# Kernel tuning notes

Hardware: AMD Instinct MI355X
Metric: run time of the kernel (lower is better)

Reference implementation:

```python
import jax, jax.numpy as jnp
import numpy as np

N_NODES = 100000
N_EDGES = 800000
D_IN = 128
D_HID = 128


def setup_inputs() -> dict:
    key = jax.random.key(0)
    ks = jax.random.split(key, 5)
    x = jax.random.normal(ks[0], (N_NODES, D_IN), dtype=jnp.float32)
    edge_index = jax.random.randint(ks[1], (2, N_EDGES), 0, N_NODES, dtype=jnp.int64)
    W1 = jax.random.normal(ks[2], (D_HID, D_IN), dtype=jnp.float32) * 0.05
    b1 = jnp.zeros((D_HID,), dtype=jnp.float32)
    W2 = jax.random.normal(ks[3], (D_HID, D_HID), dtype=jnp.float32) * 0.05
    b2 = jnp.zeros((D_HID,), dtype=jnp.float32)
    return {"x": x, "edge_index": edge_index, "W1": W1, "b1": b1, "W2": W2, "b2": b2}


def _gcn_conv(x, W, b, src, dst, norm, num_nodes):
    # x' = x @ W^T, then scatter-add normalized messages to dst, then + bias
    h = x @ W.T                                  # [N, d_out]
    msg = h[src] * norm[:, None]                 # [E+N, d_out] gather + scale
    out = jax.ops.segment_sum(msg, dst, num_segments=num_nodes)
    return out + b


def reference(x, edge_index, W1, b1, W2, b2):
    n = x.shape[0]
    loops = jnp.arange(n, dtype=edge_index.dtype)
    src = jnp.concatenate([edge_index[0], loops])  # self-loops appended (PyG GCNConv)
    dst = jnp.concatenate([edge_index[1], loops])
    # symmetric normalization: deg over target nodes (weight 1 per edge)
    deg = jax.ops.segment_sum(jnp.ones_like(dst, dtype=x.dtype), dst, num_segments=n)
    dis = jnp.where(deg > 0, jax.lax.rsqrt(jnp.maximum(deg, 1e-12)), 0.0)
    norm = dis[src] * dis[dst]
    h = jax.nn.relu(_gcn_conv(x, W1, b1, src, dst, norm, n))
    return _gcn_conv(h, W2, b2, src, dst, norm, n)
```

## Files before the change

kernel.cpp:

```cpp
#include <hip/hip_runtime.h>

#define D 128
#define BE 4096
#define SC 5120
#define LROW 136

typedef __attribute__((ext_vector_type(8))) short bf16x8;
typedef __attribute__((ext_vector_type(4))) float f32x4;
typedef __attribute__((ext_vector_type(8))) unsigned short u16x8;

__device__ inline unsigned short f2bf(float f) {
    unsigned u = __float_as_uint(f);
    return (unsigned short)((u + 0x7fff + ((u >> 16) & 1)) >> 16);
}
__device__ inline float bf2f(unsigned short s) {
    return __uint_as_float((unsigned)s << 16);
}
__device__ inline bf16x8 cvt8(const float* __restrict__ p) {
    float4 a = *(const float4*)p;
    float4 b = *(const float4*)(p + 4);
    bf16x8 r;
    r[0] = (short)f2bf(a.x); r[1] = (short)f2bf(a.y);
    r[2] = (short)f2bf(a.z); r[3] = (short)f2bf(a.w);
    r[4] = (short)f2bf(b.x); r[5] = (short)f2bf(b.y);
    r[6] = (short)f2bf(b.z); r[7] = (short)f2bf(b.w);
    return r;
}

__global__ void k_prep(const float* __restrict__ W1, const float* __restrict__ W2,
                       unsigned short* __restrict__ Wb1, unsigned short* __restrict__ Wb2,
                       int* __restrict__ bcnt, int* __restrict__ gcnt, int NBK) {
    int i = blockIdx.x * 256 + threadIdx.x;
    if (i < D * D) { Wb1[i] = f2bf(W1[i]); Wb2[i] = f2bf(W2[i]); }
    if (i < NBK) bcnt[i] = 0;
    if (i == D * D) *gcnt = 0;
}


__device__ inline void gemm1_tile(const float* __restrict__ xx,
                                  const unsigned short* __restrict__ Wb,
                                  unsigned short* __restrict__ g,
                                  int N, int tile, int t) {
    int w = t >> 6, l = t & 63;
    int r16 = l & 15, g4 = l >> 4;
    int base = tile * 128 + w * 32;
    int row0 = base + r16, row1 = row0 + 16;
    int cr0 = (row0 < N) ? row0 : N - 1;
    int cr1 = (row1 < N) ? row1 : N - 1;

    f32x4 acc0[8] = {};
    f32x4 acc1[8] = {};
    const unsigned short* wr = Wb + r16 * D + g4 * 8;

#pragma unroll 1
    for (int ks = 0; ks < 4; ks++) {
        bf16x8 b0 = cvt8(xx + (size_t)cr0 * D + g4 * 8 + ks * 32);
        bf16x8 b1 = cvt8(xx + (size_t)cr1 * D + g4 * 8 + ks * 32);
#pragma unroll
        for (int jt = 0; jt < 8; jt++) {
            bf16x8 a = *(const bf16x8*)(wr + jt * 16 * D + ks * 32);
            acc0[jt] = __builtin_amdgcn_mfma_f32_16x16x32_bf16(a, b0, acc0[jt], 0, 0, 0);
            acc1[jt] = __builtin_amdgcn_mfma_f32_16x16x32_bf16(a, b1, acc1[jt], 0, 0, 0);
        }
    }
#pragma unroll
    for (int tt = 0; tt < 2; tt++) {
        int row = base + tt * 16 + r16;
        if (row < N) {
#pragma unroll
            for (int jt = 0; jt < 8; jt++) {
                f32x4 a = tt ? acc1[jt] : acc0[jt];
                ushort4 o = { f2bf(a[0]), f2bf(a[1]), f2bf(a[2]), f2bf(a[3]) };
                *(ushort4*)&g[(size_t)row * D + jt * 16 + g4 * 4] = o;
            }
        }
    }
}


__global__ __launch_bounds__(256) void k_sort_gemm1a(
        const int* __restrict__ ei, int* __restrict__ bcnt, unsigned* __restrict__ brec,
        const float* __restrict__ x, const unsigned short* __restrict__ Wb1,
        unsigned short* __restrict__ g, int N, int E, int ntA, int sortB, int NBK) {
    int bid = blockIdx.x;
    if (bid % 3 == 2) {
        __shared__ unsigned srt[BE];
        __shared__ unsigned char bko[BE];
        __shared__ int hist[256];
        __shared__ int pfx[256];
        __shared__ int gbase[256];
        __shared__ int cur[256];
        int f = bid / 3;
        if (f >= sortB) return;
        int t = threadIdx.x;
        int e0 = f * BE;
        int n = E - e0; if (n > BE) n = BE;
        hist[t] = 0; cur[t] = 0;
        __syncthreads();
        unsigned rec[16]; int mb[16];
#pragma unroll
        for (int j = 0; j < 16; j++) {
            int e = e0 + j * 256 + t;
            if (e < E) {
                int s = ei[e], d = ei[E + e];
                rec[j] = ((unsigned)s << 9) | (unsigned)(d & 511);
                mb[j] = d >> 9;
                atomicAdd(&hist[mb[j]], 1);
            } else mb[j] = -1;
        }
        __syncthreads();
        int v = hist[t];
        pfx[t] = v;
        __syncthreads();
        for (int dd = 1; dd < 256; dd <<= 1) {
            int xv = (t >= dd) ? pfx[t - dd] : 0;
            __syncthreads();
            pfx[t] += xv;
            __syncthreads();
        }
        pfx[t] -= v;
        if (v > 0 && t < NBK) gbase[t] = atomicAdd(&bcnt[t], v);
        __syncthreads();
#pragma unroll
        for (int j = 0; j < 16; j++) {
            if (mb[j] >= 0) {
                int p = pfx[mb[j]] + atomicAdd(&cur[mb[j]], 1);
                srt[p] = rec[j];
                bko[p] = (unsigned char)mb[j];
            }
        }
        __syncthreads();
        for (int i = t; i < n; i += 256) {
            int b = bko[i];
            int pos = gbase[b] + (i - pfx[b]);
            if (pos < SC) brec[(size_t)b * SC + pos] = srt[i];
        }
    } else {
        int gid = (bid / 3) * 2 + (bid % 3);
        if (gid >= ntA) return;
        gemm1_tile(x, Wb1, g, N, gid, threadIdx.x);
    }
}

__global__ __launch_bounds__(256) void k_build_gemm1b(
        const int* __restrict__ bcnt, const unsigned* __restrict__ brec,
        int* __restrict__ cnt, int* __restrict__ rp, int* __restrict__ col,
        int* __restrict__ gcnt,
        const float* __restrict__ x, const unsigned short* __restrict__ Wb1,
        unsigned short* __restrict__ g, int N, int ntA, int ntiles, int NBK) {
    int bid = blockIdx.x;
    if (bid % 3 == 2) {
        __shared__ int c512[512];
        __shared__ int base512[512];
        __shared__ int psc[256];
        __shared__ int bksum;
        int b = bid / 3, t = threadIdx.x;
        if (b >= NBK) return;
        c512[t] = 0; c512[t + 256] = 0;
        __syncthreads();
        int total = bcnt[b]; if (total > SC) total = SC;
        for (int i = t; i < total; i += 256)
            atomicAdd(&c512[brec[(size_t)b * SC + i] & 511], 1);
        __syncthreads();
        int d0 = c512[2 * t], d1 = c512[2 * t + 1];
        int pair = d0 + d1;
        psc[t] = pair;
        __syncthreads();
        for (int dd = 1; dd < 256; dd <<= 1) {
            int xv = (t >= dd) ? psc[t - dd] : 0;
            __syncthreads();
            psc[t] += xv;
            __syncthreads();
        }
        int pexc = psc[t] - pair;
        if (t == 255) bksum = atomicAdd(gcnt, psc[255]);
        __syncthreads();
        int gb = bksum;
        base512[2 * t]     = gb + pexc;
        base512[2 * t + 1] = gb + pexc + d0;
        c512[2 * t] = 0; c512[2 * t + 1] = 0;
        __syncthreads();
        for (int i = t; i < total; i += 256) {
            unsigned rec = brec[(size_t)b * SC + i];
            int dl = rec & 511;
            int p = atomicAdd(&c512[dl], 1);
            col[base512[dl] + p] = (int)(rec >> 9);
        }
        __syncthreads();
#pragma unroll
        for (int k = 0; k < 2; k++) {
            int dl = t + k * 256;
            int node = b * 512 + dl;
            if (node < N) { cnt[node] = c512[dl]; rp[node] = base512[dl]; }
        }
    } else {
        int gid = ntA + (bid / 3) * 2 + (bid % 3);
        if (gid >= ntiles) return;
        gemm1_tile(x, Wb1, g, N, gid, threadIdx.x);
    }
}


__global__ __launch_bounds__(256) void k_agg1_g2(
        const unsigned short* __restrict__ gtab, const int* __restrict__ cnt,
        const int* __restrict__ rp, const int* __restrict__ col,
        const float* __restrict__ b1, const unsigned short* __restrict__ Wb2,
        unsigned short* __restrict__ g2, int N) {
    __shared__ __align__(16) unsigned short hl[16 * LROW];
    int t = threadIdx.x, grp = t >> 4, l16 = t & 15;
    int n0 = blockIdx.x * 16;
    int node = n0 + grp;
    bool valid = (node < N);
    int nc = valid ? node : N - 1;
    const u16x8* G = (const u16x8*)gtab;

    int deg = valid ? cnt[node] : 0;
    float disv = rsqrtf((float)(deg + 1));
    float acc[8];
    {
        u16x8 s = G[(size_t)nc * 16 + l16];
#pragma unroll
        for (int j = 0; j < 8; j++) acc[j] = bf2f(s[j]) * disv;
    }
    const int* cb = col + (valid ? rp[node] : 0);
    int i = 0;
    for (; i + 3 < deg; i += 4) {
        int u0 = cb[i], u1 = cb[i + 1], u2 = cb[i + 2], u3 = cb[i + 3];
        u16x8 m0 = G[(size_t)u0 * 16 + l16];
        u16x8 m1 = G[(size_t)u1 * 16 + l16];
        u16x8 m2 = G[(size_t)u2 * 16 + l16];
        u16x8 m3 = G[(size_t)u3 * 16 + l16];
        float d0 = rsqrtf((float)(cnt[u0] + 1));
        float d1 = rsqrtf((float)(cnt[u1] + 1));
        float d2 = rsqrtf((float)(cnt[u2] + 1));
        float d3 = rsqrtf((float)(cnt[u3] + 1));
#pragma unroll
        for (int j = 0; j < 8; j++)
            acc[j] += (bf2f(m0[j]) * d0 + bf2f(m1[j]) * d1)
                    + (bf2f(m2[j]) * d2 + bf2f(m3[j]) * d3);
    }
    for (; i < deg; i++) {
        int u = cb[i];
        u16x8 m = G[(size_t)u * 16 + l16];
        float du = rsqrtf((float)(cnt[u] + 1));
#pragma unroll
        for (int j = 0; j < 8; j++) acc[j] += bf2f(m[j]) * du;
    }
    {
        const float4* B4 = (const float4*)b1;
        float4 bb0 = B4[l16 * 2], bb1 = B4[l16 * 2 + 1];
        float r[8];
        r[0] = fmaf(acc[0], disv, bb0.x); r[1] = fmaf(acc[1], disv, bb0.y);
        r[2] = fmaf(acc[2], disv, bb0.z); r[3] = fmaf(acc[3], disv, bb0.w);
        r[4] = fmaf(acc[4], disv, bb1.x); r[5] = fmaf(acc[5], disv, bb1.y);
        r[6] = fmaf(acc[6], disv, bb1.z); r[7] = fmaf(acc[7], disv, bb1.w);
        u16x8 hv;
#pragma unroll
        for (int j = 0; j < 8; j++)
            hv[j] = valid ? f2bf(fmaxf(r[j], 0.f)) : (unsigned short)0;
        *(u16x8*)&hl[grp * LROW + l16 * 8] = hv;
    }
    __syncthreads();

    int w = t >> 6, l = t & 63;
    int r16 = l & 15, g4 = l >> 4;
    f32x4 a0 = {}, a1 = {};
    const unsigned short* wr = Wb2 + r16 * D + g4 * 8;
    int xb = r16 * LROW + g4 * 8;
#pragma unroll 1
    for (int ks = 0; ks < 4; ks++) {
        bf16x8 b = *(const bf16x8*)&hl[xb + ks * 32];
        bf16x8 A0 = *(const bf16x8*)(wr + (2 * w) * 16 * D + ks * 32);
        bf16x8 A1 = *(const bf16x8*)(wr + (2 * w + 1) * 16 * D + ks * 32);
        a0 = __builtin_amdgcn_mfma_f32_16x16x32_bf16(A0, b, a0, 0, 0, 0);
        a1 = __builtin_amdgcn_mfma_f32_16x16x32_bf16(A1, b, a1, 0, 0, 0);
    }
    int orow = n0 + r16;
    if (orow < N) {
        float dv = rsqrtf((float)(cnt[orow] + 1));
        ushort4 o0 = { f2bf(a0[0] * dv), f2bf(a0[1] * dv),
                       f2bf(a0[2] * dv), f2bf(a0[3] * dv) };
        ushort4 o1 = { f2bf(a1[0] * dv), f2bf(a1[1] * dv),
                       f2bf(a1[2] * dv), f2bf(a1[3] * dv) };
        *(ushort4*)&g2[(size_t)orow * D + (2 * w) * 16 + g4 * 4] = o0;
        *(ushort4*)&g2[(size_t)orow * D + (2 * w + 1) * 16 + g4 * 4] = o1;
    }
}

__global__ __launch_bounds__(256) void k_agg2(
        const unsigned short* __restrict__ g2, const int* __restrict__ cnt,
        const int* __restrict__ rp, const int* __restrict__ col,
        const float* __restrict__ b2, float* __restrict__ out, int N) {
    int node = blockIdx.x * 16 + (threadIdx.x >> 4);
    if (node >= N) return;
    int l16 = threadIdx.x & 15;
    const u16x8* G = (const u16x8*)g2;
    int deg = cnt[node];
    float acc[8];
    {
        u16x8 s = G[(size_t)node * 16 + l16];
#pragma unroll
        for (int j = 0; j < 8; j++) acc[j] = bf2f(s[j]);
    }
    const int* cb = col + rp[node];
    int i = 0;
    for (; i + 3 < deg; i += 4) {
        int u0 = cb[i], u1 = cb[i + 1], u2 = cb[i + 2], u3 = cb[i + 3];
        u16x8 m0 = G[(size_t)u0 * 16 + l16];
        u16x8 m1 = G[(size_t)u1 * 16 + l16];
        u16x8 m2 = G[(size_t)u2 * 16 + l16];
        u16x8 m3 = G[(size_t)u3 * 16 + l16];
#pragma unroll
        for (int j = 0; j < 8; j++)
            acc[j] += (bf2f(m0[j]) + bf2f(m1[j])) + (bf2f(m2[j]) + bf2f(m3[j]));
    }
    for (; i < deg; i++) {
        u16x8 m = G[(size_t)cb[i] * 16 + l16];
#pragma unroll
        for (int j = 0; j < 8; j++) acc[j] += bf2f(m[j]);
    }
    float disv = rsqrtf((float)(deg + 1));
    const float4* B4 = (const float4*)b2;
    float4 bb0 = B4[l16 * 2], bb1 = B4[l16 * 2 + 1];
    float4 o0, o1;
    o0.x = fmaf(acc[0], disv, bb0.x); o0.y = fmaf(acc[1], disv, bb0.y);
    o0.z = fmaf(acc[2], disv, bb0.z); o0.w = fmaf(acc[3], disv, bb0.w);
    o1.x = fmaf(acc[4], disv, bb1.x); o1.y = fmaf(acc[5], disv, bb1.y);
    o1.z = fmaf(acc[6], disv, bb1.z); o1.w = fmaf(acc[7], disv, bb1.w);
    ((float4*)out)[(size_t)node * 32 + l16 * 2]     = o0;
    ((float4*)out)[(size_t)node * 32 + l16 * 2 + 1] = o1;
}


extern "C" void kernel_launch(void* const* d_in, const int* in_sizes, int n_in,
                              void* d_out, int out_size, void* d_ws, size_t ws_size,
                              hipStream_t stream) {
    const float* x  = (const float*)d_in[0];
    const int*   ei = (const int*)d_in[1];
    const float* W1 = (const float*)d_in[2];
    const float* b1 = (const float*)d_in[3];
    const float* W2 = (const float*)d_in[4];
    const float* b2 = (const float*)d_in[5];
    float* out = (float*)d_out;

    int N = in_sizes[0] / D;
    int E = in_sizes[1] / 2;
    int NBK = (N + 511) >> 9;

    char* w = (char*)d_ws;
    unsigned short* g  = (unsigned short*)w;  size_t off = (size_t)N * D * 2;
    off = (off + 255) & ~(size_t)255;
    unsigned short* g2 = (unsigned short*)(w + off); off += (size_t)N * D * 2;
    off = (off + 255) & ~(size_t)255;
    int* cnt  = (int*)(w + off);             off += (size_t)N * 4;
    off = (off + 255) & ~(size_t)255;
    int* rp   = (int*)(w + off);             off += (size_t)N * 4;
    off = (off + 255) & ~(size_t)255;
    int* col  = (int*)(w + off);             off += (size_t)E * 4;
    off = (off + 255) & ~(size_t)255;
    unsigned short* Wb1 = (unsigned short*)(w + off); off += (size_t)D * D * 2;
    unsigned short* Wb2 = (unsigned short*)(w + off); off += (size_t)D * D * 2;
    off = (off + 255) & ~(size_t)255;
    int* bcnt = (int*)(w + off);             off += (size_t)NBK * 4;
    off = (off + 255) & ~(size_t)255;
    int* gcnt = (int*)(w + off);             off += 256;
    unsigned* brec = (unsigned*)(w + off);   off += (size_t)NBK * SC * 4;

    int ntiles = (N + 127) / 128;
    int ntA = (ntiles + 1) / 2;
    int ntB = ntiles - ntA;
    int sortB = (E + BE - 1) / BE;
    int fb1 = sortB > (ntA + 1) / 2 ? sortB : (ntA + 1) / 2;
    int fb2 = NBK   > (ntB + 1) / 2 ? NBK   : (ntB + 1) / 2;
    int agg_grid = (N + 15) / 16;

    k_prep<<<(D * D + 511) / 256, 256, 0, stream>>>(W1, W2, Wb1, Wb2, bcnt, gcnt, NBK);

    k_sort_gemm1a<<<3 * fb1, 256, 0, stream>>>(ei, bcnt, brec, x, Wb1, g,
                                               N, E, ntA, sortB, NBK);
    k_build_gemm1b<<<3 * fb2, 256, 0, stream>>>(bcnt, brec, cnt, rp, col, gcnt,
                                                x, Wb1, g, N, ntA, ntiles, NBK);

    k_agg1_g2<<<agg_grid, 256, 0, stream>>>(g, cnt, rp, col, b1, Wb2, g2, N);

    k_agg2<<<agg_grid, 256, 0, stream>>>(g2, cnt, rp, col, b2, out, N);
}
```

Measured before the change: 160.0 us.

## Sort nodes by degree for first aggregation and move whole GEMM1 into sort kernel

```diff
diff --git a/kernel.cpp b/kernel.cpp
--- a/kernel.cpp
+++ b/kernel.cpp
@@ -29,68 +29,59 @@
 
 __global__ void k_prep(const float* __restrict__ W1, const float* __restrict__ W2,
                        unsigned short* __restrict__ Wb1, unsigned short* __restrict__ Wb2,
-                       int* __restrict__ bcnt, int* __restrict__ gcnt, int NBK) {
+                       int* __restrict__ bcnt, int* __restrict__ gcnt,
+                       int* __restrict__ dbins, int NBK) {
     int i = blockIdx.x * 256 + threadIdx.x;
     if (i < D * D) { Wb1[i] = f2bf(W1[i]); Wb2[i] = f2bf(W2[i]); }
     if (i < NBK) bcnt[i] = 0;
     if (i == D * D) *gcnt = 0;
-}
-
-
-__device__ inline void gemm1_tile(const float* __restrict__ xx,
-                                  const unsigned short* __restrict__ Wb,
-                                  unsigned short* __restrict__ g,
-                                  int N, int tile, int t) {
+    if (i < 32) dbins[i] = 0;
+}
+
+
+__device__ inline void gemm1_tile64(const float* __restrict__ xx,
+                                    const unsigned short* __restrict__ Wb,
+                                    unsigned short* __restrict__ g,
+                                    int N, int tile, int t) {
     int w = t >> 6, l = t & 63;
     int r16 = l & 15, g4 = l >> 4;
-    int base = tile * 128 + w * 32;
-    int row0 = base + r16, row1 = row0 + 16;
-    int cr0 = (row0 < N) ? row0 : N - 1;
-    int cr1 = (row1 < N) ? row1 : N - 1;
-
-    f32x4 acc0[8] = {};
-    f32x4 acc1[8] = {};
+    int row = tile * 64 + w * 16 + r16;
+    int cr = (row < N) ? row : N - 1;
+    f32x4 acc[8] = {};
     const unsigned short* wr = Wb + r16 * D + g4 * 8;
-
 #pragma unroll 1
     for (int ks = 0; ks < 4; ks++) {
-        bf16x8 b0 = cvt8(xx + (size_t)cr0 * D + g4 * 8 + ks * 32);
-        bf16x8 b1 = cvt8(xx + (size_t)cr1 * D + g4 * 8 + ks * 32);
+        bf16x8 b = cvt8(xx + (size_t)cr * D + g4 * 8 + ks * 32);
 #pragma unroll
         for (int jt = 0; jt < 8; jt++) {
             bf16x8 a = *(const bf16x8*)(wr + jt * 16 * D + ks * 32);
-            acc0[jt] = __builtin_amdgcn_mfma_f32_16x16x32_bf16(a, b0, acc0[jt], 0, 0, 0);
-            acc1[jt] = __builtin_amdgcn_mfma_f32_16x16x32_bf16(a, b1, acc1[jt], 0, 0, 0);
-        }
-    }
-#pragma unroll
-    for (int tt = 0; tt < 2; tt++) {
-        int row = base + tt * 16 + r16;
-        if (row < N) {
-#pragma unroll
-            for (int jt = 0; jt < 8; jt++) {
-                f32x4 a = tt ? acc1[jt] : acc0[jt];
-                ushort4 o = { f2bf(a[0]), f2bf(a[1]), f2bf(a[2]), f2bf(a[3]) };
-                *(ushort4*)&g[(size_t)row * D + jt * 16 + g4 * 4] = o;
-            }
-        }
-    }
-}
-
-
-__global__ __launch_bounds__(256) void k_sort_gemm1a(
+            acc[jt] = __builtin_amdgcn_mfma_f32_16x16x32_bf16(a, b, acc[jt], 0, 0, 0);
+        }
+    }
+    if (row < N) {
+#pragma unroll
+        for (int jt = 0; jt < 8; jt++) {
+            ushort4 o = { f2bf(acc[jt][0]), f2bf(acc[jt][1]),
+                          f2bf(acc[jt][2]), f2bf(acc[jt][3]) };
+            *(ushort4*)&g[(size_t)row * D + jt * 16 + g4 * 4] = o;
+        }
+    }
+}
+
+
+__global__ __launch_bounds__(256) void k_sort_gemm1(
         const int* __restrict__ ei, int* __restrict__ bcnt, unsigned* __restrict__ brec,
         const float* __restrict__ x, const unsigned short* __restrict__ Wb1,
-        unsigned short* __restrict__ g, int N, int E, int ntA, int sortB, int NBK) {
+        unsigned short* __restrict__ g, int N, int E, int nt64, int sortB, int NBK) {
     int bid = blockIdx.x;
-    if (bid % 3 == 2) {
+    if (bid % 9 == 8) {
         __shared__ unsigned srt[BE];
         __shared__ unsigned char bko[BE];
         __shared__ int hist[256];
         __shared__ int pfx[256];
         __shared__ int gbase[256];
         __shared__ int cur[256];
-        int f = bid / 3;
+        int f = bid / 9;
         if (f >= sortB) return;
         int t = threadIdx.x;
         int e0 = f * BE;
@@ -136,67 +127,105 @@
             if (pos < SC) brec[(size_t)b * SC + pos] = srt[i];
         }
     } else {
-        int gid = (bid / 3) * 2 + (bid % 3);
-        if (gid >= ntA) return;
-        gemm1_tile(x, Wb1, g, N, gid, threadIdx.x);
-    }
-}
-
-__global__ __launch_bounds__(256) void k_build_gemm1b(
-        const int* __restrict__ bcnt, const unsigned* __restrict__ brec,
-        int* __restrict__ cnt, int* __restrict__ rp, int* __restrict__ col,
-        int* __restrict__ gcnt,
-        const float* __restrict__ x, const unsigned short* __restrict__ Wb1,
-        unsigned short* __restrict__ g, int N, int ntA, int ntiles, int NBK) {
-    int bid = blockIdx.x;
-    if (bid % 3 == 2) {
-        __shared__ int c512[512];
-        __shared__ int base512[512];
-        __shared__ int psc[256];
-        __shared__ int bksum;
-        int b = bid / 3, t = threadIdx.x;
-        if (b >= NBK) return;
-        c512[t] = 0; c512[t + 256] = 0;
-        __syncthreads();
-        int total = bcnt[b]; if (total > SC) total = SC;
-        for (int i = t; i < total; i += 256)
-            atomicAdd(&c512[brec[(size_t)b * SC + i] & 511], 1);
-        __syncthreads();
-        int d0 = c512[2 * t], d1 = c512[2 * t + 1];
-        int pair = d0 + d1;
-        psc[t] = pair;
-        __syncthreads();
-        for (int dd = 1; dd < 256; dd <<= 1) {
-            int xv = (t >= dd) ? psc[t - dd] : 0;
-            __syncthreads();
-            psc[t] += xv;
-            __syncthreads();
-        }
-        int pexc = psc[t] - pair;
-        if (t == 255) bksum = atomicAdd(gcnt, psc[255]);
-        __syncthreads();
-        int gb = bksum;
-        base512[2 * t]     = gb + pexc;
-        base512[2 * t + 1] = gb + pexc + d0;
-        c512[2 * t] = 0; c512[2 * t + 1] = 0;
-        __syncthreads();
-        for (int i = t; i < total; i += 256) {
-            unsigned rec = brec[(size_t)b * SC + i];
-            int dl = rec & 511;
-            int p = atomicAdd(&c512[dl], 1);
-            col[base512[dl] + p] = (int)(rec >> 9);
-        }
-        __syncthreads();
-#pragma unroll
-        for (int k = 0; k < 2; k++) {
-            int dl = t + k * 256;
-            int node = b * 512 + dl;
-            if (node < N) { cnt[node] = c512[dl]; rp[node] = base512[dl]; }
-        }
-    } else {
-        int gid = ntA + (bid / 3) * 2 + (bid % 3);
-        if (gid >= ntiles) return;
-        gemm1_tile(x, Wb1, g, N, gid, threadIdx.x);
+        int gid = (bid / 9) * 8 + (bid % 9);
+        if (gid >= nt64) return;
+        gemm1_tile64(x, Wb1, g, N, gid, threadIdx.x);
+    }
+}
+
+__global__ __launch_bounds__(256) void k_build(const int* __restrict__ bcnt,
+                                               const unsigned* __restrict__ brec,
+                                               int* __restrict__ cnt,
+                                               int* __restrict__ rp,
+                                               int* __restrict__ col,
+                                               int* __restrict__ gcnt,
+                                               int* __restrict__ dbins, int N) {
+    __shared__ int c512[512];
+    __shared__ int base512[512];
+    __shared__ int psc[256];
+    __shared__ int dh[32];
+    __shared__ int bksum;
+    int b = blockIdx.x, t = threadIdx.x;
+    c512[t] = 0; c512[t + 256] = 0;
+    if (t < 32) dh[t] = 0;
+    __syncthreads();
+    int total = bcnt[b]; if (total > SC) total = SC;
+    for (int i = t; i < total; i += 256)
+        atomicAdd(&c512[brec[(size_t)b * SC + i] & 511], 1);
+    __syncthreads();
+    int d0 = c512[2 * t], d1 = c512[2 * t + 1];
+    int pair = d0 + d1;
+    psc[t] = pair;
+    __syncthreads();
+    for (int dd = 1; dd < 256; dd <<= 1) {
+        int xv = (t >= dd) ? psc[t - dd] : 0;
+        __syncthreads();
+        psc[t] += xv;
+        __syncthreads();
+    }
+    int pexc = psc[t] - pair;
+    if (t == 255) bksum = atomicAdd(gcnt, psc[255]);
+    __syncthreads();
+    int gb = bksum;
+    base512[2 * t]     = gb + pexc;
+    base512[2 * t + 1] = gb + pexc + d0;
+    c512[2 * t] = 0; c512[2 * t + 1] = 0;
+    __syncthreads();
+    for (int i = t; i < total; i += 256) {
+        unsigned rec = brec[(size_t)b * SC + i];
+        int dl = rec & 511;
+        int p = atomicAdd(&c512[dl], 1);
+        col[base512[dl] + p] = (int)(rec >> 9);
+    }
+    __syncthreads();
+#pragma unroll
+    for (int k = 0; k < 2; k++) {
+        int dl = t + k * 256;
+        int node = b * 512 + dl;
+        if (node < N) {
+            int dg = c512[dl];
+            cnt[node] = dg; rp[node] = base512[dl];
+            atomicAdd(&dh[dg > 31 ? 31 : dg], 1);
+        }
+    }
+    __syncthreads();
+    if (t < 32 && dh[t] > 0) atomicAdd(&dbins[t], dh[t]);
+}
+
+__global__ void k_scan32(int* __restrict__ dbins) {
+    if (threadIdx.x == 0) {
+        int run = 0;
+        for (int i = 0; i < 32; i++) { int v = dbins[i]; dbins[i] = run; run += v; }
+    }
+}
+
+
+__global__ __launch_bounds__(256) void k_scatter(const int* __restrict__ cnt,
+                                                 int* __restrict__ dbins,
+                                                 int* __restrict__ perm, int N) {
+    __shared__ int lh[32], lbase[32], lcur[32];
+    int b = blockIdx.x, t = threadIdx.x;
+    if (t < 32) { lh[t] = 0; lcur[t] = 0; }
+    __syncthreads();
+    int bin[2];
+#pragma unroll
+    for (int k = 0; k < 2; k++) {
+        int node = b * 512 + k * 256 + t;
+        if (node < N) {
+            int d = cnt[node];
+            bin[k] = d > 31 ? 31 : d;
+            atomicAdd(&lh[bin[k]], 1);
+        } else bin[k] = -1;
+    }
+    __syncthreads();
+    if (t < 32 && lh[t] > 0) lbase[t] = atomicAdd(&dbins[t], lh[t]);
+    __syncthreads();
+#pragma unroll
+    for (int k = 0; k < 2; k++) {
+        if (bin[k] >= 0) {
+            int r = atomicAdd(&lcur[bin[k]], 1);
+            perm[lbase[bin[k]] + r] = b * 512 + k * 256 + t;
+        }
     }
 }
 
@@ -204,21 +233,22 @@
 __global__ __launch_bounds__(256) void k_agg1_g2(
         const unsigned short* __restrict__ gtab, const int* __restrict__ cnt,
         const int* __restrict__ rp, const int* __restrict__ col,
+        const int* __restrict__ perm,
         const float* __restrict__ b1, const unsigned short* __restrict__ Wb2,
         unsigned short* __restrict__ g2, int N) {
     __shared__ __align__(16) unsigned short hl[16 * LROW];
     int t = threadIdx.x, grp = t >> 4, l16 = t & 15;
     int n0 = blockIdx.x * 16;
-    int node = n0 + grp;
-    bool valid = (node < N);
-    int nc = valid ? node : N - 1;
+    int pos = n0 + grp;
+    bool valid = (pos < N);
+    int node = valid ? perm[pos] : 0;
     const u16x8* G = (const u16x8*)gtab;
 
     int deg = valid ? cnt[node] : 0;
     float disv = rsqrtf((float)(deg + 1));
     float acc[8];
     {
-        u16x8 s = G[(size_t)nc * 16 + l16];
+        u16x8 s = G[(size_t)node * 16 + l16];
 #pragma unroll
         for (int j = 0; j < 8; j++) acc[j] = bf2f(s[j]) * disv;
     }
@@ -275,8 +305,9 @@
         a0 = __builtin_amdgcn_mfma_f32_16x16x32_bf16(A0, b, a0, 0, 0, 0);
         a1 = __builtin_amdgcn_mfma_f32_16x16x32_bf16(A1, b, a1, 0, 0, 0);
     }
-    int orow = n0 + r16;
-    if (orow < N) {
+    int pos2 = n0 + r16;
+    if (pos2 < N) {
+        int orow = perm[pos2];
         float dv = rsqrtf((float)(cnt[orow] + 1));
         ushort4 o0 = { f2bf(a0[0] * dv), f2bf(a0[1] * dv),
                        f2bf(a0[2] * dv), f2bf(a0[3] * dv) };
@@ -356,6 +387,8 @@
     off = (off + 255) & ~(size_t)255;
     int* rp   = (int*)(w + off);             off += (size_t)N * 4;
     off = (off + 255) & ~(size_t)255;
+    int* perm = (int*)(w + off);             off += (size_t)N * 4;
+    off = (off + 255) & ~(size_t)255;
     int* col  = (int*)(w + off);             off += (size_t)E * 4;
     off = (off + 255) & ~(size_t)255;
     unsigned short* Wb1 = (unsigned short*)(w + off); off += (size_t)D * D * 2;
@@ -364,24 +397,23 @@
     int* bcnt = (int*)(w + off);             off += (size_t)NBK * 4;
     off = (off + 255) & ~(size_t)255;
     int* gcnt = (int*)(w + off);             off += 256;
+    int* dbins = (int*)(w + off);            off += 256;
     unsigned* brec = (unsigned*)(w + off);   off += (size_t)NBK * SC * 4;
 
-    int ntiles = (N + 127) / 128;
-    int ntA = (ntiles + 1) / 2;
-    int ntB = ntiles - ntA;
+    int nt64 = (N + 63) / 64;
     int sortB = (E + BE - 1) / BE;
-    int fb1 = sortB > (ntA + 1) / 2 ? sortB : (ntA + 1) / 2;
-    int fb2 = NBK   > (ntB + 1) / 2 ? NBK   : (ntB + 1) / 2;
+    int fb = sortB > (nt64 + 7) / 8 ? sortB : (nt64 + 7) / 8;
     int agg_grid = (N + 15) / 16;
 
-    k_prep<<<(D * D + 511) / 256, 256, 0, stream>>>(W1, W2, Wb1, Wb2, bcnt, gcnt, NBK);
-
-    k_sort_gemm1a<<<3 * fb1, 256, 0, stream>>>(ei, bcnt, brec, x, Wb1, g,
-                                               N, E, ntA, sortB, NBK);
-    k_build_gemm1b<<<3 * fb2, 256, 0, stream>>>(bcnt, brec, cnt, rp, col, gcnt,
-                                                x, Wb1, g, N, ntA, ntiles, NBK);
-
-    k_agg1_g2<<<agg_grid, 256, 0, stream>>>(g, cnt, rp, col, b1, Wb2, g2, N);
+    k_prep<<<(D * D + 511) / 256, 256, 0, stream>>>(W1, W2, Wb1, Wb2, bcnt, gcnt, dbins, NBK);
+
+    k_sort_gemm1<<<9 * fb, 256, 0, stream>>>(ei, bcnt, brec, x, Wb1, g,
+                                             N, E, nt64, sortB, NBK);
+    k_build<<<NBK, 256, 0, stream>>>(bcnt, brec, cnt, rp, col, gcnt, dbins, N);
+    k_scan32<<<1, 64, 0, stream>>>(dbins);
+    k_scatter<<<NBK, 256, 0, stream>>>(cnt, dbins, perm, N);
+
+    k_agg1_g2<<<agg_grid, 256, 0, stream>>>(g, cnt, rp, col, perm, b1, Wb2, g2, N);
 
     k_agg2<<<agg_grid, 256, 0, stream>>>(g2, cnt, rp, col, b2, out, N);
 }
```

After: 169.1 us. +5.6%, slower.

## Run all GEMM1 tiles alongside edge sort; make CSR build its own kernel

Applied to the files above, without the earlier changes.

```diff
diff --git a/kernel.cpp b/kernel.cpp
--- a/kernel.cpp
+++ b/kernel.cpp
@@ -78,19 +78,19 @@
 }
 
 
-__global__ __launch_bounds__(256) void k_sort_gemm1a(
+__global__ __launch_bounds__(256) void k_sort_gemm1(
         const int* __restrict__ ei, int* __restrict__ bcnt, unsigned* __restrict__ brec,
         const float* __restrict__ x, const unsigned short* __restrict__ Wb1,
-        unsigned short* __restrict__ g, int N, int E, int ntA, int sortB, int NBK) {
+        unsigned short* __restrict__ g, int N, int E, int ntiles, int sortB, int NBK) {
     int bid = blockIdx.x;
-    if (bid % 3 == 2) {
+    if (bid % 9 == 8) {
         __shared__ unsigned srt[BE];
         __shared__ unsigned char bko[BE];
         __shared__ int hist[256];
         __shared__ int pfx[256];
         __shared__ int gbase[256];
         __shared__ int cur[256];
-        int f = bid / 3;
+        int f = bid / 9;
         if (f >= sortB) return;
         int t = threadIdx.x;
         int e0 = f * BE;
@@ -136,67 +136,59 @@
             if (pos < SC) brec[(size_t)b * SC + pos] = srt[i];
         }
     } else {
-        int gid = (bid / 3) * 2 + (bid % 3);
-        if (gid >= ntA) return;
-        gemm1_tile(x, Wb1, g, N, gid, threadIdx.x);
-    }
-}
-
-__global__ __launch_bounds__(256) void k_build_gemm1b(
-        const int* __restrict__ bcnt, const unsigned* __restrict__ brec,
-        int* __restrict__ cnt, int* __restrict__ rp, int* __restrict__ col,
-        int* __restrict__ gcnt,
-        const float* __restrict__ x, const unsigned short* __restrict__ Wb1,
-        unsigned short* __restrict__ g, int N, int ntA, int ntiles, int NBK) {
-    int bid = blockIdx.x;
-    if (bid % 3 == 2) {
-        __shared__ int c512[512];
-        __shared__ int base512[512];
-        __shared__ int psc[256];
-        __shared__ int bksum;
-        int b = bid / 3, t = threadIdx.x;
-        if (b >= NBK) return;
-        c512[t] = 0; c512[t + 256] = 0;
-        __syncthreads();
-        int total = bcnt[b]; if (total > SC) total = SC;
-        for (int i = t; i < total; i += 256)
-            atomicAdd(&c512[brec[(size_t)b * SC + i] & 511], 1);
-        __syncthreads();
-        int d0 = c512[2 * t], d1 = c512[2 * t + 1];
-        int pair = d0 + d1;
-        psc[t] = pair;
-        __syncthreads();
-        for (int dd = 1; dd < 256; dd <<= 1) {
-            int xv = (t >= dd) ? psc[t - dd] : 0;
-            __syncthreads();
-            psc[t] += xv;
-            __syncthreads();
-        }
-        int pexc = psc[t] - pair;
-        if (t == 255) bksum = atomicAdd(gcnt, psc[255]);
-        __syncthreads();
-        int gb = bksum;
-        base512[2 * t]     = gb + pexc;
-        base512[2 * t + 1] = gb + pexc + d0;
-        c512[2 * t] = 0; c512[2 * t + 1] = 0;
-        __syncthreads();
-        for (int i = t; i < total; i += 256) {
-            unsigned rec = brec[(size_t)b * SC + i];
-            int dl = rec & 511;
-            int p = atomicAdd(&c512[dl], 1);
-            col[base512[dl] + p] = (int)(rec >> 9);
-        }
-        __syncthreads();
-#pragma unroll
-        for (int k = 0; k < 2; k++) {
-            int dl = t + k * 256;
-            int node = b * 512 + dl;
-            if (node < N) { cnt[node] = c512[dl]; rp[node] = base512[dl]; }
-        }
-    } else {
-        int gid = ntA + (bid / 3) * 2 + (bid % 3);
+        int gid = (bid / 9) * 8 + (bid % 9);
         if (gid >= ntiles) return;
         gemm1_tile(x, Wb1, g, N, gid, threadIdx.x);
+    }
+}
+
+__global__ __launch_bounds__(256) void k_build(const int* __restrict__ bcnt,
+                                               const unsigned* __restrict__ brec,
+                                               int* __restrict__ cnt,
+                                               int* __restrict__ rp,
+                                               int* __restrict__ col,
+                                               int* __restrict__ gcnt, int N) {
+    __shared__ int c512[512];
+    __shared__ int base512[512];
+    __shared__ int psc[256];
+    __shared__ int bksum;
+    int b = blockIdx.x, t = threadIdx.x;
+    c512[t] = 0; c512[t + 256] = 0;
+    __syncthreads();
+    int total = bcnt[b]; if (total > SC) total = SC;
+    for (int i = t; i < total; i += 256)
+        atomicAdd(&c512[brec[(size_t)b * SC + i] & 511], 1);
+    __syncthreads();
+    int d0 = c512[2 * t], d1 = c512[2 * t + 1];
+    int pair = d0 + d1;
+    psc[t] = pair;
+    __syncthreads();
+    for (int dd = 1; dd < 256; dd <<= 1) {
+        int xv = (t >= dd) ? psc[t - dd] : 0;
+        __syncthreads();
+        psc[t] += xv;
+        __syncthreads();
+    }
+    int pexc = psc[t] - pair;
+    if (t == 255) bksum = atomicAdd(gcnt, psc[255]);
+    __syncthreads();
+    int gb = bksum;
+    base512[2 * t]     = gb + pexc;
+    base512[2 * t + 1] = gb + pexc + d0;
+    c512[2 * t] = 0; c512[2 * t + 1] = 0;
+    __syncthreads();
+    for (int i = t; i < total; i += 256) {
+        unsigned rec = brec[(size_t)b * SC + i];
+        int dl = rec & 511;
+        int p = atomicAdd(&c512[dl], 1);
+        col[base512[dl] + p] = (int)(rec >> 9);
+    }
+    __syncthreads();
+#pragma unroll
+    for (int k = 0; k < 2; k++) {
+        int dl = t + k * 256;
+        int node = b * 512 + dl;
+        if (node < N) { cnt[node] = c512[dl]; rp[node] = base512[dl]; }
     }
 }
 
@@ -367,19 +359,15 @@
     unsigned* brec = (unsigned*)(w + off);   off += (size_t)NBK * SC * 4;
 
     int ntiles = (N + 127) / 128;
-    int ntA = (ntiles + 1) / 2;
-    int ntB = ntiles - ntA;
-    int sortB = (E + BE - 1) / BE;
-    int fb1 = sortB > (ntA + 1) / 2 ? sortB : (ntA + 1) / 2;
-    int fb2 = NBK   > (ntB + 1) / 2 ? NBK   : (ntB + 1) / 2;
+    int sortB  = (E + BE - 1) / BE;
+    int fb = sortB > (ntiles + 7) / 8 ? sortB : (ntiles + 7) / 8;
     int agg_grid = (N + 15) / 16;
 
     k_prep<<<(D * D + 511) / 256, 256, 0, stream>>>(W1, W2, Wb1, Wb2, bcnt, gcnt, NBK);
 
-    k_sort_gemm1a<<<3 * fb1, 256, 0, stream>>>(ei, bcnt, brec, x, Wb1, g,
-                                               N, E, ntA, sortB, NBK);
-    k_build_gemm1b<<<3 * fb2, 256, 0, stream>>>(bcnt, brec, cnt, rp, col, gcnt,
-                                                x, Wb1, g, N, ntA, ntiles, NBK);
+    k_sort_gemm1<<<9 * fb, 256, 0, stream>>>(ei, bcnt, brec, x, Wb1, g,
+                                             N, E, ntiles, sortB, NBK);
+    k_build<<<NBK, 256, 0, stream>>>(bcnt, brec, cnt, rp, col, gcnt, N);
 
     k_agg1_g2<<<agg_grid, 256, 0, stream>>>(g, cnt, rp, col, b1, Wb2, g2, N);
 
```

Result: faster. 154.6 us, median of 2 (-3.4%).
